# Performance work log

Measured on AMD Instinct MI355X. Metric: run time of the kernel, lower is better.

The kernel has to match this reference:

```python
import jax, jax.numpy as jnp
import numpy as np

N1, N2, F = 512, 512, 128
H = 512  # hidden width


def _xavier(key, shape):
    fan_in, fan_out = shape
    std = (2.0 / (fan_in + fan_out)) ** 0.5
    return jax.random.normal(key, shape, dtype=jnp.float32) * std


def setup_inputs() -> dict:
    key = jax.random.key(0)
    ks = jax.random.split(key, 8)
    V1 = jax.random.normal(ks[0], (1, N1, F), dtype=jnp.float32)
    V2 = jax.random.normal(ks[1], (1, N2, F), dtype=jnp.float32)
    W1 = _xavier(ks[2], (2 * F, H))
    b1 = 0.0001 + 5e-05 * jax.random.normal(ks[3], (H,), dtype=jnp.float32)
    W2 = _xavier(ks[4], (H, H))
    b2 = 0.0001 + 5e-05 * jax.random.normal(ks[5], (H,), dtype=jnp.float32)
    W3 = _xavier(ks[6], (H, 2))
    b3 = 0.0001 + 5e-05 * jax.random.normal(ks[7], (2,), dtype=jnp.float32)
    return {"V1": V1, "V2": V2, "W1": W1, "b1": b1, "W2": W2, "b2": b2, "W3": W3, "b3": b3}


def reference(V1, V2, W1, b1, W2, b2, W3, b3):
    n1, n2, f = V1.shape[1], V2.shape[1], V1.shape[2]
    # Fused broadcast-concat replacing the N1*N2 Python double loop
    # (i outer, j inner; V1[i] first, V2[j] second -> row-major reshape matches stack order)
    pairs = jnp.concatenate([
        jnp.broadcast_to(V1[0][:, None, :], (n1, n2, f)),
        jnp.broadcast_to(V2[0][None, :, :], (n1, n2, f)),
    ], axis=-1).reshape(1, n1 * n2, 2 * f)
    h = jax.nn.relu(pairs @ W1 + b1)
    h = jax.nn.relu(h @ W2 + b2)
    out = jax.nn.relu(h @ W3 + b3)  # final LinearEmbedding also has ReLU by default
    return out
```

## Files before the change

kernel.cpp:

```cpp
#include <hip/hip_runtime.h>


typedef short bf16x8 __attribute__((ext_vector_type(8)));
typedef float f32x16 __attribute__((ext_vector_type(16)));

#define NROW 512
#define FDIM 128
#define HDIM 512

__device__ __forceinline__ unsigned int pk2(float x, float y) {
  unsigned int r;
  asm("v_cvt_pk_bf16_f32 %0, %1, %2" : "=v"(r) : "v"(x), "v"(y));
  return r;
}
__device__ __forceinline__ unsigned short f2bf(float x) {
  unsigned int u = __builtin_bit_cast(unsigned int, x);
  u += 0x7fffu + ((u >> 16) & 1u);
  return (unsigned short)(u >> 16);
}
__device__ __forceinline__ float bflo(unsigned int u) {
  return __builtin_bit_cast(float, u << 16);
}
__device__ __forceinline__ float bfhi(unsigned int u) {
  return __builtin_bit_cast(float, u & 0xffff0000u);
}

__global__ __launch_bounds__(256) void prep_ab(
    const float* __restrict__ V1, const float* __restrict__ V2,
    const float* __restrict__ W1, const float* __restrict__ b1,
    float* __restrict__ Ap, unsigned short* __restrict__ Bpb) {
  __shared__ float sv[4 * FDIM];
  const int b = blockIdx.x;
  const int t = threadIdx.x;
  const bool isB = b >= 128;
  const int r0 = (b & 127) * 4;
  const float* V = isB ? V2 : V1;
  const float* W = W1 + (isB ? FDIM * HDIM : 0);
  for (int idx = t; idx < 4 * FDIM; idx += 256) sv[idx] = V[r0 * FDIM + idx];
  __syncthreads();
  float s[4][2] = {};
  for (int k = 0; k < FDIM; ++k) {
    const float w0 = W[k * HDIM + t];
    const float w1 = W[k * HDIM + t + 256];
#pragma unroll
    for (int r = 0; r < 4; ++r) {
      const float v = sv[r * FDIM + k];
      s[r][0] += v * w0;
      s[r][1] += v * w1;
    }
  }
  if (isB) {
#pragma unroll
    for (int r = 0; r < 4; ++r) {
      Bpb[(r0 + r) * HDIM + t] = f2bf(s[r][0]);
      Bpb[(r0 + r) * HDIM + t + 256] = f2bf(s[r][1]);
    }
  } else {
    const float bb0 = b1[t];
    const float bb1 = b1[t + 256];
#pragma unroll
    for (int r = 0; r < 4; ++r) {
      Ap[(r0 + r) * HDIM + t] = s[r][0] + bb0;
      Ap[(r0 + r) * HDIM + t + 256] = s[r][1] + bb1;
    }
  }
}

__global__ __launch_bounds__(256) void prep_w2(const float* __restrict__ W2,
                                               unsigned short* __restrict__ W2T) {
  const int o = blockIdx.x * 256 + threadIdx.x;
  const int kc = o >> 9;
  const int n = o & 511;
  unsigned int u[4];
#pragma unroll
  for (int e2 = 0; e2 < 4; ++e2)
    u[e2] = pk2(W2[(kc * 8 + 2 * e2) * HDIM + n], W2[(kc * 8 + 2 * e2 + 1) * HDIM + n]);
  *(uint4*)(W2T + (size_t)o * 8) = make_uint4(u[0], u[1], u[2], u[3]);
}

__global__ __launch_bounds__(512, 2) void mlp_main(
    const float* __restrict__ Ap, const unsigned short* __restrict__ Bpb,
    const unsigned short* __restrict__ W2T, const float* __restrict__ b2,
    const float* __restrict__ W3, const float* __restrict__ b3,
    float* __restrict__ out) {
  extern __shared__ char smem[];
  char* sA = smem;

  const int tid = threadIdx.x;
  const int wave = tid >> 6;
  const int lane = tid & 63;
  const int cl = lane & 31;
  const int hi = lane >> 5;
  const int r15 = lane & 15;

  const int m0 = blockIdx.x * 128;
  const int i = m0 >> 9;
  const int j0 = m0 & 511;

  const char* bbase = (const char*)W2T + (((wave << 6) + cl) << 4) + (hi << 13);

  bf16x8 af[3][4], bfr[5][2];
#pragma unroll
  for (int q = 0; q < 4; ++q) {
    const char* bp = bbase + ((size_t)q << 14);
    bfr[q][0] = *(const bf16x8*)(bp);
    bfr[q][1] = *(const bf16x8*)(bp + (1 << 9));
  }
  float w30[2], w31[2], bb[2];
#pragma unroll
  for (int nt = 0; nt < 2; ++nt) {
    const int n = (wave << 6) + (nt << 5) + cl;
    w30[nt] = W3[2 * n];
    w31[nt] = W3[2 * n + 1];
    bb[nt] = b2[n];
  }
  const float bb3_0 = b3[0], bb3_1 = b3[1];

  {
    const int c = tid & 63;
    const int rsub = tid >> 6;
    const float4 a0 = *(const float4*)(Ap + i * HDIM + c * 8);
    const float4 a1 = *(const float4*)(Ap + i * HDIM + c * 8 + 4);
#pragma unroll
    for (int it = 0; it < 16; ++it) {
      const int row = it * 8 + rsub;
      const uint4 ub = *(const uint4*)(Bpb + (size_t)(j0 + row) * HDIM + c * 8);
      const uint4 v = make_uint4(
          pk2(fmaxf(a0.x + bflo(ub.x), 0.f), fmaxf(a0.y + bfhi(ub.x), 0.f)),
          pk2(fmaxf(a0.z + bflo(ub.y), 0.f), fmaxf(a0.w + bfhi(ub.y), 0.f)),
          pk2(fmaxf(a1.x + bflo(ub.z), 0.f), fmaxf(a1.y + bfhi(ub.z), 0.f)),
          pk2(fmaxf(a1.z + bflo(ub.w), 0.f), fmaxf(a1.w + bfhi(ub.w), 0.f)));
      *(uint4*)(sA + row * 1024 + ((c ^ (row & 15)) << 4)) = v;
    }
  }
  __syncthreads();

  f32x16 acc[4][2];
#pragma unroll
  for (int mt = 0; mt < 4; ++mt)
#pragma unroll
    for (int nt = 0; nt < 2; ++nt)
#pragma unroll
      for (int q = 0; q < 16; ++q) acc[mt][nt][q] = 0.f;

  const char* abase0 = sA + cl * 1024;
  {
#pragma unroll
    for (int q = 0; q < 2; ++q) {
      const int off = (((q << 1) | hi) ^ r15) << 4;
#pragma unroll
      for (int mt = 0; mt < 4; ++mt)
        af[q][mt] = *(const bf16x8*)(abase0 + mt * 32768 + off);
    }
  }
#pragma unroll
  for (int s = 0; s < 32; ++s) {
    if (s < 30) {
      const int off = ((((s + 2) << 1) | hi) ^ r15) << 4;
#pragma unroll
      for (int mt = 0; mt < 4; ++mt)
        af[(s + 2) % 3][mt] = *(const bf16x8*)(abase0 + mt * 32768 + off);
    }
    if (s < 28) {
      const char* bp = bbase + ((size_t)(s + 4) << 14);
      bfr[(s + 4) % 5][0] = *(const bf16x8*)(bp);
      bfr[(s + 4) % 5][1] = *(const bf16x8*)(bp + (1 << 9));
    }
    __builtin_amdgcn_s_setprio(1);
#pragma unroll
    for (int nt = 0; nt < 2; ++nt)
#pragma unroll
      for (int mt = 0; mt < 4; ++mt)
        acc[mt][nt] = __builtin_amdgcn_mfma_f32_32x32x16_bf16(af[s % 3][mt], bfr[s % 5][nt],
                                                              acc[mt][nt], 0, 0, 0);
    __builtin_amdgcn_s_setprio(0);
  }

  __syncthreads();

#pragma unroll
  for (int rnd = 0; rnd < 2; ++rnd) {
#pragma unroll
    for (int ml = 0; ml < 2; ++ml) {
      const int mt = rnd * 2 + ml;
      char* ebuf = smem + ml * 65536;
#pragma unroll
      for (int rp = 0; rp < 8; ++rp) {
        const int ra = 2 * rp;
        const float h0a = fmaxf(acc[mt][0][ra] + bb[0], 0.f);
        const float h1a = fmaxf(acc[mt][1][ra] + bb[1], 0.f);
        const float h0b = fmaxf(acc[mt][0][ra + 1] + bb[0], 0.f);
        const float h1b = fmaxf(acc[mt][1][ra + 1] + bb[1], 0.f);
        const float4 v =
            make_float4(h0a * w30[0] + h1a * w30[1], h0a * w31[0] + h1a * w31[1],
                        h0b * w30[0] + h1b * w30[1], h0b * w31[0] + h1b * w31[1]);
        const int rpi = ((ra & 3) + 8 * (ra >> 2) + 4 * hi) >> 1;
        *(float4*)(ebuf + rpi * 4096 + (((wave << 5) + cl) << 4)) = v;
      }
    }
    __syncthreads();
    {
      const int ml = tid >> 8;
      const int t2 = tid & 255;
      const int rpi = t2 >> 4;
      const int sub = t2 & 15;
      const char* ebuf = smem + ml * 65536;
      float4 s4 = make_float4(0.f, 0.f, 0.f, 0.f);
#pragma unroll
      for (int k = 0; k < 16; ++k) {
        const float4 v = *(const float4*)(ebuf + rpi * 4096 + ((sub + (k << 4)) << 4));
        s4.x += v.x; s4.y += v.y; s4.z += v.z; s4.w += v.w;
      }
#pragma unroll
      for (int d = 1; d < 16; d <<= 1) {
        s4.x += __shfl_xor(s4.x, d, 64);
        s4.y += __shfl_xor(s4.y, d, 64);
        s4.z += __shfl_xor(s4.z, d, 64);
        s4.w += __shfl_xor(s4.w, d, 64);
      }
      if (sub == 0) {
        const int rg = m0 + ((rnd * 2 + ml) << 5) + (rpi << 1);
        *(float4*)(out + rg * 2) =
            make_float4(fmaxf(s4.x + bb3_0, 0.f), fmaxf(s4.y + bb3_1, 0.f),
                        fmaxf(s4.z + bb3_0, 0.f), fmaxf(s4.w + bb3_1, 0.f));
      }
    }
    __syncthreads();
  }
}

extern "C" void kernel_launch(void* const* d_in, const int* in_sizes, int n_in,
                              void* d_out, int out_size, void* d_ws, size_t ws_size,
                              hipStream_t stream) {
  const float* V1 = (const float*)d_in[0];
  const float* V2 = (const float*)d_in[1];
  const float* W1 = (const float*)d_in[2];
  const float* b1 = (const float*)d_in[3];
  const float* W2 = (const float*)d_in[4];
  const float* b2 = (const float*)d_in[5];
  const float* W3 = (const float*)d_in[6];
  const float* b3 = (const float*)d_in[7];

  float* Ap = (float*)d_ws;
  unsigned short* Bpb = (unsigned short*)(Ap + NROW * HDIM);
  unsigned short* W2T = Bpb + NROW * HDIM;

  const int smem_bytes = 131072;
  (void)hipFuncSetAttribute((const void*)mlp_main,
                            hipFuncAttributeMaxDynamicSharedMemorySize, smem_bytes);

  prep_ab<<<256, 256, 0, stream>>>(V1, V2, W1, b1, Ap, Bpb);
  prep_w2<<<128, 256, 0, stream>>>(W2, W2T);
  mlp_main<<<2048, 512, smem_bytes, stream>>>(Ap, Bpb, W2T, b2, W3, b3, (float*)d_out);
}
```

Measured before the change: 144.6 us.

## Double-buffer K-chunked A and W2 tiles in LDS with async global-to-LDS loads

Restructures the main MLP GEMM to loop over K in 8 chunks of 64. Each chunk's W2T slice is staged into LDS via asynchronous global_load_lds, and the relu(A+B) activation chunk is built into a double-buffered LDS tile while MFMAs run on the current chunk. This replaces the previous design of building the full A tile upfront and streaming B fragments straight from global memory. It raises LDS use to 160KB per block, likely cutting occupancy to one block per CU, and adds a block barrier per chunk.

```diff
diff --git a/kernel.cpp b/kernel.cpp
--- a/kernel.cpp
+++ b/kernel.cpp
@@ -84,28 +84,19 @@
     const float* __restrict__ W3, const float* __restrict__ b3,
     float* __restrict__ out) {
   extern __shared__ char smem[];
-  char* sA = smem;
 
   const int tid = threadIdx.x;
   const int wave = tid >> 6;
   const int lane = tid & 63;
   const int cl = lane & 31;
   const int hi = lane >> 5;
-  const int r15 = lane & 15;
+  const int frow = tid >> 2;
+  const int fc2 = (tid & 3) << 1;
 
   const int m0 = blockIdx.x * 128;
   const int i = m0 >> 9;
   const int j0 = m0 & 511;
 
-  const char* bbase = (const char*)W2T + (((wave << 6) + cl) << 4) + (hi << 13);
-
-  bf16x8 af[3][4], bfr[5][2];
-#pragma unroll
-  for (int q = 0; q < 4; ++q) {
-    const char* bp = bbase + ((size_t)q << 14);
-    bfr[q][0] = *(const bf16x8*)(bp);
-    bfr[q][1] = *(const bf16x8*)(bp + (1 << 9));
-  }
   float w30[2], w31[2], bb[2];
 #pragma unroll
   for (int nt = 0; nt < 2; ++nt) {
@@ -116,22 +107,37 @@
   }
   const float bb3_0 = b3[0], bb3_1 = b3[1];
 
+  const int a_cl7 = cl & 7;
+  const int bcol = ((wave << 6) + cl) << 4;
+
   {
-    const int c = tid & 63;
-    const int rsub = tid >> 6;
-    const float4 a0 = *(const float4*)(Ap + i * HDIM + c * 8);
-    const float4 a1 = *(const float4*)(Ap + i * HDIM + c * 8 + 4);
-#pragma unroll
-    for (int it = 0; it < 16; ++it) {
-      const int row = it * 8 + rsub;
-      const uint4 ub = *(const uint4*)(Bpb + (size_t)(j0 + row) * HDIM + c * 8);
-      const uint4 v = make_uint4(
-          pk2(fmaxf(a0.x + bflo(ub.x), 0.f), fmaxf(a0.y + bfhi(ub.x), 0.f)),
-          pk2(fmaxf(a0.z + bflo(ub.y), 0.f), fmaxf(a0.w + bfhi(ub.y), 0.f)),
-          pk2(fmaxf(a1.x + bflo(ub.z), 0.f), fmaxf(a1.y + bfhi(ub.z), 0.f)),
-          pk2(fmaxf(a1.z + bflo(ub.w), 0.f), fmaxf(a1.w + bfhi(ub.w), 0.f)));
-      *(uint4*)(sA + row * 1024 + ((c ^ (row & 15)) << 4)) = v;
-    }
+    const int kh = fc2 * 8;
+    const uint4 ub0 = *(const uint4*)(Bpb + (size_t)(j0 + frow) * HDIM + kh);
+    const uint4 ub1 = *(const uint4*)(Bpb + (size_t)(j0 + frow) * HDIM + kh + 8);
+    const float4 fa0 = *(const float4*)(Ap + i * HDIM + kh);
+    const float4 fa1 = *(const float4*)(Ap + i * HDIM + kh + 4);
+    const float4 fa2 = *(const float4*)(Ap + i * HDIM + kh + 8);
+    const float4 fa3 = *(const float4*)(Ap + i * HDIM + kh + 12);
+#pragma unroll
+    for (int it = 0; it < 8; ++it) {
+      const int off = (it * 512 + tid) * 16;
+      __builtin_amdgcn_global_load_lds(
+          (const __attribute__((address_space(1))) void*)((const char*)W2T + off),
+          (__attribute__((address_space(3))) void*)(smem + off), 16, 0, 0);
+    }
+    const uint4 v0 = make_uint4(
+        pk2(fmaxf(fa0.x + bflo(ub0.x), 0.f), fmaxf(fa0.y + bfhi(ub0.x), 0.f)),
+        pk2(fmaxf(fa0.z + bflo(ub0.y), 0.f), fmaxf(fa0.w + bfhi(ub0.y), 0.f)),
+        pk2(fmaxf(fa1.x + bflo(ub0.z), 0.f), fmaxf(fa1.y + bfhi(ub0.z), 0.f)),
+        pk2(fmaxf(fa1.z + bflo(ub0.w), 0.f), fmaxf(fa1.w + bfhi(ub0.w), 0.f)));
+    const uint4 v1 = make_uint4(
+        pk2(fmaxf(fa2.x + bflo(ub1.x), 0.f), fmaxf(fa2.y + bfhi(ub1.x), 0.f)),
+        pk2(fmaxf(fa2.z + bflo(ub1.y), 0.f), fmaxf(fa2.w + bfhi(ub1.y), 0.f)),
+        pk2(fmaxf(fa3.x + bflo(ub1.z), 0.f), fmaxf(fa3.y + bfhi(ub1.z), 0.f)),
+        pk2(fmaxf(fa3.z + bflo(ub1.w), 0.f), fmaxf(fa3.w + bfhi(ub1.w), 0.f)));
+    char* sA0 = smem + 131072;
+    *(uint4*)(sA0 + frow * 128 + ((fc2 ^ (frow & 7)) << 4)) = v0;
+    *(uint4*)(sA0 + frow * 128 + (((fc2 + 1) ^ (frow & 7)) << 4)) = v1;
   }
   __syncthreads();
 
@@ -143,40 +149,83 @@
 #pragma unroll
       for (int q = 0; q < 16; ++q) acc[mt][nt][q] = 0.f;
 
-  const char* abase0 = sA + cl * 1024;
-  {
-#pragma unroll
-    for (int q = 0; q < 2; ++q) {
-      const int off = (((q << 1) | hi) ^ r15) << 4;
+#pragma unroll 1
+  for (int e = 0; e < 8; ++e) {
+    char* sBc = smem + (e & 1) * 65536;
+    char* sAc = smem + 131072 + (e & 1) * 16384;
+    char* sBn = smem + ((e & 1) ^ 1) * 65536;
+    char* sAn = smem + 131072 + ((e & 1) ^ 1) * 16384;
+
+    uint4 ub0, ub1;
+    float4 fa0, fa1, fa2, fa3;
+    if (e < 7) {
+      const int kh = (e + 1) * 64 + fc2 * 8;
+      ub0 = *(const uint4*)(Bpb + (size_t)(j0 + frow) * HDIM + kh);
+      ub1 = *(const uint4*)(Bpb + (size_t)(j0 + frow) * HDIM + kh + 8);
+      fa0 = *(const float4*)(Ap + i * HDIM + kh);
+      fa1 = *(const float4*)(Ap + i * HDIM + kh + 4);
+      fa2 = *(const float4*)(Ap + i * HDIM + kh + 8);
+      fa3 = *(const float4*)(Ap + i * HDIM + kh + 12);
+      const char* gsrc = (const char*)W2T + ((size_t)(e + 1) << 16);
+#pragma unroll
+      for (int it = 0; it < 8; ++it) {
+        const int off = (it * 512 + tid) * 16;
+        __builtin_amdgcn_global_load_lds(
+            (const __attribute__((address_space(1))) void*)(gsrc + off),
+            (__attribute__((address_space(3))) void*)(sBn + off), 16, 0, 0);
+      }
+    }
+
+    const char* alane = sAc + cl * 128;
+    bf16x8 af[2][4], bf[2][2];
+    {
+      const int co = (hi ^ a_cl7) << 4;
 #pragma unroll
       for (int mt = 0; mt < 4; ++mt)
-        af[q][mt] = *(const bf16x8*)(abase0 + mt * 32768 + off);
-    }
-  }
-#pragma unroll
-  for (int s = 0; s < 32; ++s) {
-    if (s < 30) {
-      const int off = ((((s + 2) << 1) | hi) ^ r15) << 4;
-#pragma unroll
-      for (int mt = 0; mt < 4; ++mt)
-        af[(s + 2) % 3][mt] = *(const bf16x8*)(abase0 + mt * 32768 + off);
-    }
-    if (s < 28) {
-      const char* bp = bbase + ((size_t)(s + 4) << 14);
-      bfr[(s + 4) % 5][0] = *(const bf16x8*)(bp);
-      bfr[(s + 4) % 5][1] = *(const bf16x8*)(bp + (1 << 9));
-    }
-    __builtin_amdgcn_s_setprio(1);
-#pragma unroll
-    for (int nt = 0; nt < 2; ++nt)
-#pragma unroll
-      for (int mt = 0; mt < 4; ++mt)
-        acc[mt][nt] = __builtin_amdgcn_mfma_f32_32x32x16_bf16(af[s % 3][mt], bfr[s % 5][nt],
-                                                              acc[mt][nt], 0, 0, 0);
-    __builtin_amdgcn_s_setprio(0);
-  }
-
-  __syncthreads();
+        af[0][mt] = *(const bf16x8*)(alane + mt * 4096 + co);
+#pragma unroll
+      for (int nt = 0; nt < 2; ++nt)
+        bf[0][nt] = *(const bf16x8*)(sBc + (hi << 13) + bcol + (nt << 9));
+    }
+#pragma unroll
+    for (int sl = 0; sl < 4; ++sl) {
+      const int cur = sl & 1;
+      if (sl < 3) {
+        const int kcl = ((sl + 1) << 1) | hi;
+        const int co = (kcl ^ a_cl7) << 4;
+#pragma unroll
+        for (int mt = 0; mt < 4; ++mt)
+          af[cur ^ 1][mt] = *(const bf16x8*)(alane + mt * 4096 + co);
+#pragma unroll
+        for (int nt = 0; nt < 2; ++nt)
+          bf[cur ^ 1][nt] = *(const bf16x8*)(sBc + (kcl << 13) + bcol + (nt << 9));
+      }
+      __builtin_amdgcn_s_setprio(1);
+#pragma unroll
+      for (int nt = 0; nt < 2; ++nt)
+#pragma unroll
+        for (int mt = 0; mt < 4; ++mt)
+          acc[mt][nt] = __builtin_amdgcn_mfma_f32_32x32x16_bf16(af[cur][mt], bf[cur][nt],
+                                                                acc[mt][nt], 0, 0, 0);
+      __builtin_amdgcn_s_setprio(0);
+    }
+
+    if (e < 7) {
+      const uint4 v0 = make_uint4(
+          pk2(fmaxf(fa0.x + bflo(ub0.x), 0.f), fmaxf(fa0.y + bfhi(ub0.x), 0.f)),
+          pk2(fmaxf(fa0.z + bflo(ub0.y), 0.f), fmaxf(fa0.w + bfhi(ub0.y), 0.f)),
+          pk2(fmaxf(fa1.x + bflo(ub0.z), 0.f), fmaxf(fa1.y + bfhi(ub0.z), 0.f)),
+          pk2(fmaxf(fa1.z + bflo(ub0.w), 0.f), fmaxf(fa1.w + bfhi(ub0.w), 0.f)));
+      const uint4 v1 = make_uint4(
+          pk2(fmaxf(fa2.x + bflo(ub1.x), 0.f), fmaxf(fa2.y + bfhi(ub1.x), 0.f)),
+          pk2(fmaxf(fa2.z + bflo(ub1.y), 0.f), fmaxf(fa2.w + bfhi(ub1.y), 0.f)),
+          pk2(fmaxf(fa3.x + bflo(ub1.z), 0.f), fmaxf(fa3.y + bfhi(ub1.z), 0.f)),
+          pk2(fmaxf(fa3.z + bflo(ub1.w), 0.f), fmaxf(fa3.w + bfhi(ub1.w), 0.f)));
+      *(uint4*)(sAn + frow * 128 + ((fc2 ^ (frow & 7)) << 4)) = v0;
+      *(uint4*)(sAn + frow * 128 + (((fc2 + 1) ^ (frow & 7)) << 4)) = v1;
+    }
+    __syncthreads();
+  }
 
 #pragma unroll
   for (int rnd = 0; rnd < 2; ++rnd) {
@@ -245,7 +294,7 @@
   unsigned short* Bpb = (unsigned short*)(Ap + NROW * HDIM);
   unsigned short* W2T = Bpb + NROW * HDIM;
 
-  const int smem_bytes = 131072;
+  const int smem_bytes = 163840;
   (void)hipFuncSetAttribute((const void*)mlp_main,
                             hipFuncAttributeMaxDynamicSharedMemorySize, smem_bytes);
 
```

Result: slower. 185.6 us (+28.3%).
